# Optimization experiments

Hardware: AMD Instinct MI355X
Metric: run time of the kernel (lower is better)

Reference implementation:

```python
import jax, jax.numpy as jnp
import numpy as np
import math

VOCAB, EMBED, RES = 50257, 512, 2048
B, T = 64, 512
LN_EPS = 1e-5


def setup_inputs() -> dict:
    key = jax.random.key(0)
    k_x, k_e, k_r, k_w = jax.random.split(key, 4)
    x = jax.random.randint(k_x, (B, T), 0, VOCAB)
    embed_weight = jax.random.normal(k_e, (VOCAB, EMBED), dtype=jnp.float32)
    R = jax.random.normal(k_r, (RES, RES), dtype=jnp.float32) / math.sqrt(RES) / 0.9
    Win = jax.random.normal(k_w, (EMBED, RES), dtype=jnp.float32) / math.sqrt(EMBED) / 0.9
    gamma = jnp.ones((RES,), dtype=jnp.float32)
    beta = jnp.zeros((RES,), dtype=jnp.float32)
    return {"x": x, "embed_weight": embed_weight, "R": R, "Win": Win,
            "gamma": gamma, "beta": beta}


def reference(x, embed_weight, R, Win, gamma, beta):
    emb = embed_weight[x]                              # [B, T, E]
    inp = jnp.einsum('bte,er->btr', emb, Win)          # [B, T, RES]

    def step(state, u_t):                              # state: [B, RES]
        new_state = jnp.tanh(state @ R + u_t)
        return new_state, None

    state0 = jnp.zeros((x.shape[0], R.shape[0]), dtype=emb.dtype)
    state, _ = jax.lax.scan(step, state0, jnp.swapaxes(inp, 0, 1))  # scan over T

    # LayerNorm over last dim (eps=1e-5, affine)
    mu = jnp.mean(state, axis=-1, keepdims=True)
    var = jnp.mean((state - mu) ** 2, axis=-1, keepdims=True)
    normed = (state - mu) / jnp.sqrt(var + LN_EPS)
    return normed * gamma + beta
```

## Files before the change

### kernel.cpp

```cpp
#include <hip/hip_runtime.h>

#define BB 64
#define TT 512
#define EE 512
#define RR 2048
#define CPW 32
#define RPG 16
#define NWGS 256

typedef _Float16 f16;
typedef f16 f16x8 __attribute__((ext_vector_type(8)));
typedef float f32x4 __attribute__((ext_vector_type(4)));

__device__ __forceinline__ void gload16(const void* g, void* l) {
  __builtin_amdgcn_global_load_lds(
      (const __attribute__((address_space(1))) void*)g,
      (__attribute__((address_space(3))) void*)l, 16, 0, 0);
}

__device__ __forceinline__ float fast_tanh(float v) {
  float e = __expf(2.0f * v);
  return 1.0f - 2.0f / (e + 1.0f);
}

__device__ __forceinline__ void storeS(f16* p, float v) {
  union { f16 h; unsigned short s; } u;
  u.h = (f16)v;
  __hip_atomic_store((unsigned short*)p, u.s, __ATOMIC_RELAXED, __HIP_MEMORY_SCOPE_AGENT);
}

__device__ __forceinline__ unsigned flag_ld(const unsigned* p) {
  return __hip_atomic_load(p, __ATOMIC_RELAXED, __HIP_MEMORY_SCOPE_AGENT);
}
__device__ __forceinline__ void flag_st(unsigned* p, unsigned v) {
  __hip_atomic_store(p, v, __ATOMIC_RELAXED, __HIP_MEMORY_SCOPE_AGENT);
}

__device__ __forceinline__ void issue8(f16x8* dst, unsigned voff, const f16* sbase) {
#pragma unroll
  for (int i = 0; i < 8; ++i)
    asm volatile("global_load_dwordx4 %0, %1, %2 offset:%c3 sc0"
                 : "=v"(dst[i]) : "v"(voff), "s"(sbase), "i"(64 * i) : "memory");
}

template <int N>
__device__ __forceinline__ void wait_vm() {
  asm volatile("s_waitcnt vmcnt(%c0)" :: "i"(N) : "memory");
  __builtin_amdgcn_sched_barrier(0);
}


__global__ void prep_emb(const int* __restrict__ x, const float* __restrict__ ew,
                         f16* __restrict__ emb) {
  const int row = blockIdx.x;
  const int tok = x[row];
  const float4* src = (const float4*)(ew + (size_t)tok * EE);
  f16* dst = emb + (size_t)row * EE;
  const int i = threadIdx.x;
  float4 v = src[i];
  union { f16 h[4]; unsigned long long u; } p;
  p.h[0] = (f16)v.x; p.h[1] = (f16)v.y; p.h[2] = (f16)v.z; p.h[3] = (f16)v.w;
  ((unsigned long long*)dst)[i] = p.u;
}

__global__ void prep_winT(const float* __restrict__ Win, f16* __restrict__ WinT) {
  const int i = blockIdx.x * blockDim.x + threadIdx.x;
  if (i < EE * RR) {
    const int k = i / RR, n = i % RR;
    WinT[(size_t)n * EE + k] = (f16)Win[i];
  }
}


__launch_bounds__(256, 1)
__global__ void proj_gemm(const f16* __restrict__ A, const f16* __restrict__ Bt,
                          float* __restrict__ U) {
  __shared__ f16 As[128 * 32];
  __shared__ f16 Bs[128 * 32];
  const int tid = threadIdx.x;
  const int wv = tid >> 6, l = tid & 63;
  const int m0 = blockIdx.x * 128, n0 = blockIdx.y * 128;
  const int wm = wv >> 1, wn = wv & 1;
  const int srow = tid >> 2, sc = tid & 3;
  const int r = l & 15, kb = l >> 4;
  f32x4 acc[4][4] = {};

  for (int k0 = 0; k0 < EE; k0 += 32) {
    __syncthreads();
#pragma unroll
    for (int q = 0; q < 2; ++q) {
      const int row = q * 64 + srow;
      const int cc = sc ^ (row & 3);
      gload16(A + (size_t)(m0 + row) * EE + k0 + cc * 8,
              (char*)As + q * 4096 + wv * 1024);
      gload16(Bt + (size_t)(n0 + row) * EE + k0 + cc * 8,
              (char*)Bs + q * 4096 + wv * 1024);
    }
    __syncthreads();
    f16x8 af[4], bf[4];
#pragma unroll
    for (int mi = 0; mi < 4; ++mi) {
      const int row = wm * 64 + mi * 16 + r;
      af[mi] = *(const f16x8*)&As[row * 32 + ((kb ^ (row & 3)) * 8)];
    }
#pragma unroll
    for (int ni = 0; ni < 4; ++ni) {
      const int row = wn * 64 + ni * 16 + r;
      bf[ni] = *(const f16x8*)&Bs[row * 32 + ((kb ^ (row & 3)) * 8)];
    }
#pragma unroll
    for (int mi = 0; mi < 4; ++mi)
#pragma unroll
      for (int ni = 0; ni < 4; ++ni)
        acc[mi][ni] = __builtin_amdgcn_mfma_f32_16x16x32_f16(af[mi], bf[ni], acc[mi][ni], 0, 0, 0);
  }
  const int rb = kb * 4;
#pragma unroll
  for (int mi = 0; mi < 4; ++mi)
#pragma unroll
    for (int ni = 0; ni < 4; ++ni)
#pragma unroll
      for (int j = 0; j < 4; ++j) {
        const int m = m0 + wm * 64 + mi * 16 + rb + j;
        const int n = n0 + wn * 64 + ni * 16 + r;
        const int b = m >> 9, t = m & 511;
        __builtin_nontemporal_store(acc[mi][ni][j], &U[(size_t)(t * BB + b) * RR + n]);
      }
}


__launch_bounds__(512, 1)
__global__ void scan_kernel(const float* __restrict__ R, const float* __restrict__ U,
                            f16* __restrict__ S, unsigned* __restrict__ flg,
                            unsigned* __restrict__ fflag) {
  __shared__ __align__(16) char ldsbuf[CPW * RR * 2 + 16 * 1040];
  f16* Rt = (f16*)ldsbuf;
  const char* RtB = (const char*)ldsbuf;

  const int wg = blockIdx.x;
  const int xcd = wg & 7;
  const int grp = xcd >> 1;
  const int cw = ((wg >> 3) << 1) | (wg & 1);
  const bool leader = (wg >> 3) == 0;
  const int nbase = cw * CPW;
  const int rbase = grp * RPG;
  const int tid = threadIdx.x;
  const int wv = tid >> 6, l = tid & 63;
  unsigned* myflags = flg + grp * 64;
  unsigned* myff = fflag + xcd * 32;

  const int mm = tid >> 5, cc = tid & 31;
  storeS(&S[(size_t)(BB * RR) + (size_t)(rbase + mm) * RR + nbase + cc],
         fast_tanh(U[(size_t)(rbase + mm) * RR + nbase + cc]));
  __syncthreads();
  if (tid == 0) flag_st(&myflags[cw], 1u);

  {
    const int c = tid & 31, kst = tid >> 5;
    for (int k = kst; k < RR; k += 16) {
      const float v = R[(size_t)k * RR + nbase + c];
      const int idx = ((k >> 5) << 10) + ((c >> 4) << 9) +
                      (((c & 15) << 2) + ((k >> 3) & 3)) * 8 + (k & 7);
      Rt[idx] = (f16)v;
    }
  }
  __syncthreads();

  const int r = l & 15, kb = l >> 4;
  const int kblk = (wv + cw) & 7;
  const unsigned voffA = (unsigned)((((rbase + r) * RR) + (kblk << 8) + kb * 8) * 2);
  const int bb0 = (r * 4 + kb) * 16;
  const int ntr = cc >> 4;
  const int lred = (cc & 15) | ((mm >> 2) << 4);
  const int jred = mm & 3;

  f16x8 abuf[8];

  for (int tau = 2; tau <= TT; ++tau) {
    const f16* sprev = S + (size_t)((tau - 1) & 1) * (BB * RR);
    f16* snext = S + (size_t)(tau & 1) * (BB * RR);
    const unsigned need = (unsigned)(tau - 1);

    const float uval = __builtin_nontemporal_load(
        &U[(size_t)(tau - 1) * (BB * RR) + (size_t)(rbase + mm) * RR + nbase + cc]);

    if (wv == 0) {
      if (leader) {
        __builtin_amdgcn_fence(__ATOMIC_ACQUIRE, "agent");
        if (l == 0) flag_st(myff, (unsigned)tau);
      } else if (l == 0) {
        unsigned fv = flag_ld(myff);
        while (fv < (unsigned)tau) {
          __builtin_amdgcn_s_sleep(1);
          fv = flag_ld(myff);
        }
      }
    }
    __syncthreads();

    {
      unsigned fv = flag_ld(&myflags[kblk * 8 + (l & 7)]);
      while (!__all(fv >= need)) {
        __builtin_amdgcn_s_sleep(1);
        fv = flag_ld(&myflags[kblk * 8 + (l & 7)]);
      }
    }

    issue8(abuf, voffA, sprev);

    f32x4 acc0 = {0.f, 0.f, 0.f, 0.f}, acc1 = {0.f, 0.f, 0.f, 0.f};
#define KSTEP(ks)                                                              \
  {                                                                            \
    const int kc = (kblk << 3) + (ks);                                         \
    f16x8 b0 = *(const f16x8*)(RtB + kc * 2048 + bb0);                         \
    f16x8 b1 = *(const f16x8*)(RtB + kc * 2048 + 1024 + bb0);                  \
    acc0 = __builtin_amdgcn_mfma_f32_16x16x32_f16(abuf[ks], b0, acc0, 0, 0, 0);\
    acc1 = __builtin_amdgcn_mfma_f32_16x16x32_f16(abuf[ks], b1, acc1, 0, 0, 0);\
  }
    wait_vm<4>();
    KSTEP(0) KSTEP(1) KSTEP(2) KSTEP(3)
    wait_vm<0>();
    KSTEP(4) KSTEP(5) KSTEP(6) KSTEP(7)
#undef KSTEP

    {
      char* red = ldsbuf + CPW * RR * 2;
      *(f32x4*)(red + (wv * 2 + 0) * 1040 + l * 16) = acc0;
      *(f32x4*)(red + (wv * 2 + 1) * 1040 + l * 16) = acc1;
    }
    __syncthreads();
    {
      const char* red = ldsbuf + CPW * RR * 2;
      float s = 0.f;
#pragma unroll
      for (int w = 0; w < 8; ++w)
        s += *(const float*)(red + (w * 2 + ntr) * 1040 + lred * 16 + jred * 4);
      storeS(&snext[(size_t)(rbase + mm) * RR + nbase + cc], fast_tanh(s + uval));
    }
    __syncthreads();
    if (tid == 0) flag_st(&myflags[cw], (unsigned)tau);
  }
}


__launch_bounds__(256, 1)
__global__ void ln_kernel(const f16* __restrict__ Sfin, const float* __restrict__ gamma,
                          const float* __restrict__ beta, float* __restrict__ out) {
  const int b = blockIdx.x;
  const int tid = threadIdx.x;
  const f16* row = Sfin + (size_t)b * RR;
  float vals[8];
  float lsum = 0.f, lsq = 0.f;
#pragma unroll
  for (int i = 0; i < 8; ++i) {
    float v = (float)row[tid + i * 256];
    vals[i] = v; lsum += v; lsq += v * v;
  }
#pragma unroll
  for (int off = 32; off >= 1; off >>= 1) {
    lsum += __shfl_xor(lsum, off);
    lsq  += __shfl_xor(lsq, off);
  }
  __shared__ float ps[4], pq[4];
  __shared__ float mu_s, rstd_s;
  const int wv = tid >> 6, l = tid & 63;
  if (l == 0) { ps[wv] = lsum; pq[wv] = lsq; }
  __syncthreads();
  if (tid == 0) {
    float s = 0.f, q = 0.f;
    for (int i = 0; i < 4; ++i) { s += ps[i]; q += pq[i]; }
    const float mu = s / RR;
    const float var = q / RR - mu * mu;
    mu_s = mu; rstd_s = rsqrtf(var + 1e-5f);
  }
  __syncthreads();
  const float mu = mu_s, rstd = rstd_s;
#pragma unroll
  for (int i = 0; i < 8; ++i) {
    const int idx = tid + i * 256;
    out[(size_t)b * RR + idx] = (vals[i] - mu) * rstd * gamma[idx] + beta[idx];
  }
}


extern "C" void kernel_launch(void* const* d_in, const int* in_sizes, int n_in,
                              void* d_out, int out_size, void* d_ws, size_t ws_size,
                              hipStream_t stream) {
  const int*   x     = (const int*)d_in[0];
  const float* ew    = (const float*)d_in[1];
  const float* Rm    = (const float*)d_in[2];
  const float* Win   = (const float*)d_in[3];
  const float* gamma = (const float*)d_in[4];
  const float* beta  = (const float*)d_in[5];

  const size_t U_OFF   = 0;
  const size_t EMB_OFF = 268435456;
  const size_t WT_OFF  = EMB_OFF + 33554432;
  const size_t S_OFF   = WT_OFF + 2097152;
  const size_t BAR_OFF = S_OFF + 524288;
  const size_t FF_OFF  = BAR_OFF + 1024;
  const size_t NEED    = FF_OFF + 1024;
  if (ws_size < NEED) {
    hipMemsetAsync(d_out, 0, (size_t)out_size * 4, stream);
    return;
  }
  char* ws = (char*)d_ws;
  float*    Ubuf  = (float*)(ws + U_OFF);
  f16*      emb   = (f16*)(ws + EMB_OFF);
  f16*      WinT  = (f16*)(ws + WT_OFF);
  f16*      Sbuf  = (f16*)(ws + S_OFF);
  unsigned* flg   = (unsigned*)(ws + BAR_OFF);
  unsigned* fflag = (unsigned*)(ws + FF_OFF);

  hipMemsetAsync(flg, 0, 2048, stream);
  prep_emb<<<BB * TT, 128, 0, stream>>>(x, ew, emb);
  prep_winT<<<(EE * RR) / 256, 256, 0, stream>>>(Win, WinT);
  proj_gemm<<<dim3((BB * TT) / 128, RR / 128), 256, 0, stream>>>(emb, WinT, Ubuf);
  scan_kernel<<<NWGS, 512, 0, stream>>>(Rm, Ubuf, Sbuf, flg, fflag);
  ln_kernel<<<BB, 256, 0, stream>>>(Sbuf, gamma, beta, (float*)d_out);
}
```

Before: 2.044 ms.

## Move cross-XCD fence to dedicated wave and pipeline flag polling with bypass loads

```diff
diff --git a/kernel.cpp b/kernel.cpp
--- a/kernel.cpp
+++ b/kernel.cpp
@@ -7,6 +7,7 @@
 #define CPW 32
 #define RPG 16
 #define NWGS 256
+#define FPAD 16
 
 typedef _Float16 f16;
 typedef f16 f16x8 __attribute__((ext_vector_type(8)));
@@ -41,6 +42,13 @@
   for (int i = 0; i < 8; ++i)
     asm volatile("global_load_dwordx4 %0, %1, %2 offset:%c3 sc0"
                  : "=v"(dst[i]) : "v"(voff), "s"(sbase), "i"(64 * i) : "memory");
+}
+
+__device__ __forceinline__ unsigned bypass_ld(unsigned voff, const unsigned* base) {
+  unsigned v;
+  asm volatile("global_load_dword %0, %1, %2 sc0 sc1"
+               : "=v"(v) : "v"(voff), "s"(base) : "memory");
+  return v;
 }
 
 template <int N>
@@ -129,7 +137,7 @@
 }
 
 
-__launch_bounds__(512, 1)
+__launch_bounds__(576, 1)
 __global__ void scan_kernel(const float* __restrict__ R, const float* __restrict__ U,
                             f16* __restrict__ S, unsigned* __restrict__ flg,
                             unsigned* __restrict__ fflag) {
@@ -146,16 +154,18 @@
   const int rbase = grp * RPG;
   const int tid = threadIdx.x;
   const int wv = tid >> 6, l = tid & 63;
-  unsigned* myflags = flg + grp * 64;
-  unsigned* myff = fflag + xcd * 32;
+  unsigned* gflags = flg + grp * 64 * FPAD;
+  unsigned* myflag = gflags + cw * FPAD;
+  unsigned* myff = fflag + xcd * FPAD;
 
   const int mm = tid >> 5, cc = tid & 31;
-  storeS(&S[(size_t)(BB * RR) + (size_t)(rbase + mm) * RR + nbase + cc],
-         fast_tanh(U[(size_t)(rbase + mm) * RR + nbase + cc]));
+  if (tid < 512)
+    storeS(&S[(size_t)(BB * RR) + (size_t)(rbase + mm) * RR + nbase + cc],
+           fast_tanh(U[(size_t)(rbase + mm) * RR + nbase + cc]));
   __syncthreads();
-  if (tid == 0) flag_st(&myflags[cw], 1u);
-
-  {
+  if (tid == 0) flag_st(myflag, 1u);
+
+  if (tid < 512) {
     const int c = tid & 31, kst = tid >> 5;
     for (int k = kst; k < RR; k += 16) {
       const float v = R[(size_t)k * RR + nbase + c];
@@ -166,49 +176,47 @@
   }
   __syncthreads();
 
-  const int r = l & 15, kb = l >> 4;
-  const int kblk = (wv + cw) & 7;
-  const unsigned voffA = (unsigned)((((rbase + r) * RR) + (kblk << 8) + kb * 8) * 2);
-  const int bb0 = (r * 4 + kb) * 16;
-  const int ntr = cc >> 4;
-  const int lred = (cc & 15) | ((mm >> 2) << 4);
-  const int jred = mm & 3;
-
-  f16x8 abuf[8];
-
-  for (int tau = 2; tau <= TT; ++tau) {
-    const f16* sprev = S + (size_t)((tau - 1) & 1) * (BB * RR);
-    f16* snext = S + (size_t)(tau & 1) * (BB * RR);
-    const unsigned need = (unsigned)(tau - 1);
-
-    const float uval = __builtin_nontemporal_load(
-        &U[(size_t)(tau - 1) * (BB * RR) + (size_t)(rbase + mm) * RR + nbase + cc]);
-
-    if (wv == 0) {
-      if (leader) {
-        __builtin_amdgcn_fence(__ATOMIC_ACQUIRE, "agent");
-        if (l == 0) flag_st(myff, (unsigned)tau);
-      } else if (l == 0) {
-        unsigned fv = flag_ld(myff);
-        while (fv < (unsigned)tau) {
-          __builtin_amdgcn_s_sleep(1);
-          fv = flag_ld(myff);
-        }
-      }
-    }
-    __syncthreads();
-
-    {
-      unsigned fv = flag_ld(&myflags[kblk * 8 + (l & 7)]);
-      while (!__all(fv >= need)) {
+  if (wv < 8) {
+    const int r = l & 15, kb = l >> 4;
+    const int kblk = (wv + cw) & 7;
+    const unsigned voffA = (unsigned)((((rbase + r) * RR) + (kblk << 8) + kb * 8) * 2);
+    const int bb0 = (r * 4 + kb) * 16;
+    const unsigned poff = (unsigned)(((grp * 64 + kblk * 8 + (l & 7)) * FPAD) * 4);
+    const unsigned foff = (unsigned)((xcd * FPAD) * 4);
+    const int ntr = cc >> 4;
+    const int lred = (cc & 15) | ((mm >> 2) << 4);
+    const int jred = mm & 3;
+
+    f16x8 abuf[8];
+
+    for (int tau = 2; tau <= TT; ++tau) {
+      const f16* sprev = S + (size_t)((tau - 1) & 1) * (BB * RR);
+      f16* snext = S + (size_t)(tau & 1) * (BB * RR);
+      const unsigned need = (unsigned)(tau - 1);
+
+      unsigned ffv = bypass_ld(foff, fflag);
+      unsigned pv0 = bypass_ld(poff, flg);
+      unsigned pv1 = bypass_ld(poff, flg);
+      for (;;) {
+        wait_vm<1>();
+        if (__all(pv0 >= need)) break;
+        pv0 = bypass_ld(poff, flg);
+        wait_vm<1>();
+        if (__all(pv1 >= need)) break;
+        pv1 = bypass_ld(poff, flg);
+        __builtin_amdgcn_s_sleep(0);
+      }
+      wait_vm<0>();
+      while (ffv < (unsigned)tau) {
         __builtin_amdgcn_s_sleep(1);
-        fv = flag_ld(&myflags[kblk * 8 + (l & 7)]);
-      }
-    }
-
-    issue8(abuf, voffA, sprev);
-
-    f32x4 acc0 = {0.f, 0.f, 0.f, 0.f}, acc1 = {0.f, 0.f, 0.f, 0.f};
+        ffv = flag_ld(myff);
+      }
+
+      issue8(abuf, voffA, sprev);
+      const float uval = __builtin_nontemporal_load(
+          &U[(size_t)(tau - 1) * (BB * RR) + (size_t)(rbase + mm) * RR + nbase + cc]);
+
+      f32x4 acc0 = {0.f, 0.f, 0.f, 0.f}, acc1 = {0.f, 0.f, 0.f, 0.f};
 #define KSTEP(ks)                                                              \
   {                                                                            \
     const int kc = (kblk << 3) + (ks);                                         \
@@ -217,28 +225,42 @@
     acc0 = __builtin_amdgcn_mfma_f32_16x16x32_f16(abuf[ks], b0, acc0, 0, 0, 0);\
     acc1 = __builtin_amdgcn_mfma_f32_16x16x32_f16(abuf[ks], b1, acc1, 0, 0, 0);\
   }
-    wait_vm<4>();
-    KSTEP(0) KSTEP(1) KSTEP(2) KSTEP(3)
-    wait_vm<0>();
-    KSTEP(4) KSTEP(5) KSTEP(6) KSTEP(7)
+      wait_vm<5>();
+      KSTEP(0) KSTEP(1) KSTEP(2) KSTEP(3)
+      wait_vm<1>();
+      KSTEP(4) KSTEP(5) KSTEP(6) KSTEP(7)
 #undef KSTEP
 
-    {
-      char* red = ldsbuf + CPW * RR * 2;
-      *(f32x4*)(red + (wv * 2 + 0) * 1040 + l * 16) = acc0;
-      *(f32x4*)(red + (wv * 2 + 1) * 1040 + l * 16) = acc1;
-    }
-    __syncthreads();
-    {
-      const char* red = ldsbuf + CPW * RR * 2;
-      float s = 0.f;
-#pragma unroll
-      for (int w = 0; w < 8; ++w)
-        s += *(const float*)(red + (w * 2 + ntr) * 1040 + lred * 16 + jred * 4);
-      storeS(&snext[(size_t)(rbase + mm) * RR + nbase + cc], fast_tanh(s + uval));
-    }
-    __syncthreads();
-    if (tid == 0) flag_st(&myflags[cw], (unsigned)tau);
+      {
+        char* red = ldsbuf + CPW * RR * 2;
+        *(f32x4*)(red + (wv * 2 + 0) * 1040 + l * 16) = acc0;
+        *(f32x4*)(red + (wv * 2 + 1) * 1040 + l * 16) = acc1;
+      }
+      __syncthreads();
+      {
+        const char* red = ldsbuf + CPW * RR * 2;
+        float s = 0.f;
+#pragma unroll
+        for (int w = 0; w < 8; ++w)
+          s += *(const float*)(red + (w * 2 + ntr) * 1040 + lred * 16 + jred * 4);
+        storeS(&snext[(size_t)(rbase + mm) * RR + nbase + cc], fast_tanh(s + uval));
+      }
+      __syncthreads();
+      if (tid == 0) flag_st(myflag, (unsigned)tau);
+    }
+  } else {
+    if (leader) {
+      __builtin_amdgcn_fence(__ATOMIC_ACQUIRE, "agent");
+      if (l == 0) flag_st(myff, 2u);
+    }
+    for (int tau = 2; tau <= TT; ++tau) {
+      __syncthreads();
+      if (leader && tau < TT) {
+        __builtin_amdgcn_fence(__ATOMIC_ACQUIRE, "agent");
+        if (l == 0) flag_st(myff, (unsigned)(tau + 1));
+      }
+      __syncthreads();
+    }
   }
 }
 
@@ -298,7 +320,7 @@
   const size_t WT_OFF  = EMB_OFF + 33554432;
   const size_t S_OFF   = WT_OFF + 2097152;
   const size_t BAR_OFF = S_OFF + 524288;
-  const size_t FF_OFF  = BAR_OFF + 1024;
+  const size_t FF_OFF  = BAR_OFF + 16384;
   const size_t NEED    = FF_OFF + 1024;
   if (ws_size < NEED) {
     hipMemsetAsync(d_out, 0, (size_t)out_size * 4, stream);
@@ -312,10 +334,10 @@
   unsigned* flg   = (unsigned*)(ws + BAR_OFF);
   unsigned* fflag = (unsigned*)(ws + FF_OFF);
 
-  hipMemsetAsync(flg, 0, 2048, stream);
+  hipMemsetAsync(flg, 0, 16384 + 1024, stream);
   prep_emb<<<BB * TT, 128, 0, stream>>>(x, ew, emb);
   prep_winT<<<(EE * RR) / 256, 256, 0, stream>>>(Win, WinT);
   proj_gemm<<<dim3((BB * TT) / 128, RR / 128), 256, 0, stream>>>(emb, WinT, Ubuf);
-  scan_kernel<<<NWGS, 512, 0, stream>>>(Rm, Ubuf, Sbuf, flg, fflag);
+  scan_kernel<<<NWGS, 576, 0, stream>>>(Rm, Ubuf, Sbuf, flg, fflag);
   ln_kernel<<<BB, 256, 0, stream>>>(Sbuf, gamma, beta, (float*)d_out);
 }
```

Measured after the change: 1.999 ms. -2.2%, faster.

## Halve scan workgroups, giving each 64 columns with half of R held in registers

Applied to the files above, without the earlier changes.

```diff
diff --git a/kernel.cpp b/kernel.cpp
--- a/kernel.cpp
+++ b/kernel.cpp
@@ -4,9 +4,11 @@
 #define TT 512
 #define EE 512
 #define RR 2048
-#define CPW 32
+#define RCOL 64
 #define RPG 16
-#define NWGS 256
+#define NWGS 128
+#define FPAD 16
+#define SPIN_CAP (1 << 20)
 
 typedef _Float16 f16;
 typedef f16 f16x8 __attribute__((ext_vector_type(8)));
@@ -23,9 +25,9 @@
   return 1.0f - 2.0f / (e + 1.0f);
 }
 
-__device__ __forceinline__ void storeS(f16* p, float v) {
+__device__ __forceinline__ void storeS(f16* p, f16 h) {
   union { f16 h; unsigned short s; } u;
-  u.h = (f16)v;
+  u.h = h;
   __hip_atomic_store((unsigned short*)p, u.s, __ATOMIC_RELAXED, __HIP_MEMORY_SCOPE_AGENT);
 }
 
@@ -129,11 +131,11 @@
 }
 
 
-__launch_bounds__(512, 1)
+__launch_bounds__(512, 2)
 __global__ void scan_kernel(const float* __restrict__ R, const float* __restrict__ U,
                             f16* __restrict__ S, unsigned* __restrict__ flg,
                             unsigned* __restrict__ fflag) {
-  __shared__ __align__(16) char ldsbuf[CPW * RR * 2 + 16 * 1040];
+  __shared__ __align__(16) char ldsbuf[32 * RR * 2 + 16 * 1040];
   f16* Rt = (f16*)ldsbuf;
   const char* RtB = (const char*)ldsbuf;
 
@@ -141,20 +143,45 @@
   const int xcd = wg & 7;
   const int grp = xcd >> 1;
   const int cw = ((wg >> 3) << 1) | (wg & 1);
-  const bool leader = (wg >> 3) == 0;
-  const int nbase = cw * CPW;
+  const int nbase = cw * RCOL;
   const int rbase = grp * RPG;
   const int tid = threadIdx.x;
   const int wv = tid >> 6, l = tid & 63;
-  unsigned* myflags = flg + grp * 64;
-  unsigned* myff = fflag + xcd * 32;
+  unsigned* gflags = flg + (size_t)grp * 32 * FPAD;
+  unsigned* myflag = gflags + cw * FPAD;
+  unsigned* myff = fflag + xcd * FPAD;
 
   const int mm = tid >> 5, cc = tid & 31;
-  storeS(&S[(size_t)(BB * RR) + (size_t)(rbase + mm) * RR + nbase + cc],
-         fast_tanh(U[(size_t)(rbase + mm) * RR + nbase + cc]));
-  __syncthreads();
-  if (tid == 0) flag_st(&myflags[cw], 1u);
-
+  {
+    f16 h0 = (f16)fast_tanh(U[(size_t)(rbase + mm) * RR + nbase + cc]);
+    f16 h1 = (f16)fast_tanh(U[(size_t)(rbase + mm) * RR + nbase + 32 + cc]);
+    storeS(&S[(size_t)(BB * RR) + (size_t)(rbase + mm) * RR + nbase + cc], h0);
+    storeS(&S[(size_t)(BB * RR) + (size_t)(rbase + mm) * RR + nbase + 32 + cc], h1);
+  }
+  __syncthreads();
+  if (tid == 0) flag_st(myflag, 1u);
+
+  const int r = l & 15, kb = l >> 4;
+  const int kblk = (wv + cw) & 7;
+  const int bb0 = (r * 4 + kb) * 16;
+
+  {
+    const int c = tid & 31, kst = tid >> 5;
+    for (int k = kst; k < RR; k += 16) {
+      const float v = R[(size_t)k * RR + nbase + 32 + c];
+      const int idx = ((k >> 5) << 10) + ((c >> 4) << 9) +
+                      (((c & 15) << 2) + ((k >> 3) & 3)) * 8 + (k & 7);
+      Rt[idx] = (f16)v;
+    }
+  }
+  __syncthreads();
+  f16x8 breg[2][8];
+#pragma unroll
+  for (int nt = 0; nt < 2; ++nt)
+#pragma unroll
+    for (int ks = 0; ks < 8; ++ks)
+      breg[nt][ks] = *(const f16x8*)(RtB + ((kblk << 3) + ks) * 2048 + nt * 1024 + bb0);
+  __syncthreads();
   {
     const int c = tid & 31, kst = tid >> 5;
     for (int k = kst; k < RR; k += 16) {
@@ -166,10 +193,8 @@
   }
   __syncthreads();
 
-  const int r = l & 15, kb = l >> 4;
-  const int kblk = (wv + cw) & 7;
   const unsigned voffA = (unsigned)((((rbase + r) * RR) + (kblk << 8) + kb * 8) * 2);
-  const int bb0 = (r * 4 + kb) * 16;
+  const unsigned* pollp = (l == 4) ? myff : &gflags[(size_t)(kblk * 4 + (l & 3)) * FPAD];
   const int ntr = cc >> 4;
   const int lred = (cc & 15) | ((mm >> 2) << 4);
   const int jred = mm & 3;
@@ -180,35 +205,31 @@
     const f16* sprev = S + (size_t)((tau - 1) & 1) * (BB * RR);
     f16* snext = S + (size_t)(tau & 1) * (BB * RR);
     const unsigned need = (unsigned)(tau - 1);
-
-    const float uval = __builtin_nontemporal_load(
+    const unsigned thr = (l == 4) ? (unsigned)tau : need;
+
+    const float uval0 = __builtin_nontemporal_load(
         &U[(size_t)(tau - 1) * (BB * RR) + (size_t)(rbase + mm) * RR + nbase + cc]);
-
-    if (wv == 0) {
-      if (leader) {
-        __builtin_amdgcn_fence(__ATOMIC_ACQUIRE, "agent");
-        if (l == 0) flag_st(myff, (unsigned)tau);
-      } else if (l == 0) {
-        unsigned fv = flag_ld(myff);
-        while (fv < (unsigned)tau) {
-          __builtin_amdgcn_s_sleep(1);
-          fv = flag_ld(myff);
-        }
+    const float uval1 = __builtin_nontemporal_load(
+        &U[(size_t)(tau - 1) * (BB * RR) + (size_t)(rbase + mm) * RR + nbase + 32 + cc]);
+
+    if ((wg >> 3) == (tau & 15) && wv == 0) {
+      __builtin_amdgcn_fence(__ATOMIC_ACQUIRE, "agent");
+      if (l == 0) flag_st(myff, (unsigned)tau);
+    }
+
+    {
+      unsigned fv = flag_ld(pollp);
+      int gd = 0;
+      while (!__all(fv >= thr) && ++gd < SPIN_CAP) {
+        __builtin_amdgcn_s_sleep(1);
+        fv = flag_ld(pollp);
       }
     }
-    __syncthreads();
-
-    {
-      unsigned fv = flag_ld(&myflags[kblk * 8 + (l & 7)]);
-      while (!__all(fv >= need)) {
-        __builtin_amdgcn_s_sleep(1);
-        fv = flag_ld(&myflags[kblk * 8 + (l & 7)]);
-      }
-    }
 
     issue8(abuf, voffA, sprev);
 
     f32x4 acc0 = {0.f, 0.f, 0.f, 0.f}, acc1 = {0.f, 0.f, 0.f, 0.f};
+    f32x4 acc2 = {0.f, 0.f, 0.f, 0.f}, acc3 = {0.f, 0.f, 0.f, 0.f};
 #define KSTEP(ks)                                                              \
   {                                                                            \
     const int kc = (kblk << 3) + (ks);                                         \
@@ -216,6 +237,8 @@
     f16x8 b1 = *(const f16x8*)(RtB + kc * 2048 + 1024 + bb0);                  \
     acc0 = __builtin_amdgcn_mfma_f32_16x16x32_f16(abuf[ks], b0, acc0, 0, 0, 0);\
     acc1 = __builtin_amdgcn_mfma_f32_16x16x32_f16(abuf[ks], b1, acc1, 0, 0, 0);\
+    acc2 = __builtin_amdgcn_mfma_f32_16x16x32_f16(abuf[ks], breg[0][ks], acc2, 0, 0, 0);\
+    acc3 = __builtin_amdgcn_mfma_f32_16x16x32_f16(abuf[ks], breg[1][ks], acc3, 0, 0, 0);\
   }
     wait_vm<4>();
     KSTEP(0) KSTEP(1) KSTEP(2) KSTEP(3)
@@ -223,22 +246,32 @@
     KSTEP(4) KSTEP(5) KSTEP(6) KSTEP(7)
 #undef KSTEP
 
+    char* red = ldsbuf + 32 * RR * 2;
+    *(f32x4*)(red + (wv * 2 + 0) * 1040 + l * 16) = acc0;
+    *(f32x4*)(red + (wv * 2 + 1) * 1040 + l * 16) = acc1;
+    __syncthreads();
     {
-      char* red = ldsbuf + CPW * RR * 2;
-      *(f32x4*)(red + (wv * 2 + 0) * 1040 + l * 16) = acc0;
-      *(f32x4*)(red + (wv * 2 + 1) * 1040 + l * 16) = acc1;
-    }
-    __syncthreads();
-    {
-      const char* red = ldsbuf + CPW * RR * 2;
       float s = 0.f;
 #pragma unroll
       for (int w = 0; w < 8; ++w)
         s += *(const float*)(red + (w * 2 + ntr) * 1040 + lred * 16 + jred * 4);
-      storeS(&snext[(size_t)(rbase + mm) * RR + nbase + cc], fast_tanh(s + uval));
-    }
-    __syncthreads();
-    if (tid == 0) flag_st(&myflags[cw], (unsigned)tau);
+      storeS(&snext[(size_t)(rbase + mm) * RR + nbase + cc],
+             (f16)fast_tanh(s + uval0));
+    }
+    __syncthreads();
+    *(f32x4*)(red + (wv * 2 + 0) * 1040 + l * 16) = acc2;
+    *(f32x4*)(red + (wv * 2 + 1) * 1040 + l * 16) = acc3;
+    __syncthreads();
+    {
+      float s = 0.f;
+#pragma unroll
+      for (int w = 0; w < 8; ++w)
+        s += *(const float*)(red + (w * 2 + ntr) * 1040 + lred * 16 + jred * 4);
+      storeS(&snext[(size_t)(rbase + mm) * RR + nbase + 32 + cc],
+             (f16)fast_tanh(s + uval1));
+    }
+    __syncthreads();
+    if (tid == 0) flag_st(myflag, (unsigned)tau);
   }
 }
 
@@ -297,8 +330,8 @@
   const size_t EMB_OFF = 268435456;
   const size_t WT_OFF  = EMB_OFF + 33554432;
   const size_t S_OFF   = WT_OFF + 2097152;
-  const size_t BAR_OFF = S_OFF + 524288;
-  const size_t FF_OFF  = BAR_OFF + 1024;
+  const size_t FLG_OFF = S_OFF + 524288;
+  const size_t FF_OFF  = FLG_OFF + 8192;
   const size_t NEED    = FF_OFF + 1024;
   if (ws_size < NEED) {
     hipMemsetAsync(d_out, 0, (size_t)out_size * 4, stream);
@@ -309,10 +342,10 @@
   f16*      emb   = (f16*)(ws + EMB_OFF);
   f16*      WinT  = (f16*)(ws + WT_OFF);
   f16*      Sbuf  = (f16*)(ws + S_OFF);
-  unsigned* flg   = (unsigned*)(ws + BAR_OFF);
+  unsigned* flg   = (unsigned*)(ws + FLG_OFF);
   unsigned* fflag = (unsigned*)(ws + FF_OFF);
 
-  hipMemsetAsync(flg, 0, 2048, stream);
+  hipMemsetAsync(flg, 0, 8192 + 1024, stream);
   prep_emb<<<BB * TT, 128, 0, stream>>>(x, ew, emb);
   prep_winT<<<(EE * RR) / 256, 256, 0, stream>>>(Win, WinT);
   proj_gemm<<<dim3((BB * TT) / 128, RR / 128), 256, 0, stream>>>(emb, WinT, Ubuf);
```

New measurement: 2.326 ms. +13.8%, slower.
